# Optimization experiments

Hardware: AMD Instinct MI355X
Metric: run time of the kernel (lower is better)

Reference implementation:

```python
import jax, jax.numpy as jnp
import numpy as np

TOKEN_SELF_ATTN_VALUE = -50000.0


def setup_inputs() -> dict:
    key = jax.random.key(0)
    k1, k2, k3 = jax.random.split(key, 3)
    batch, seqlen, dim = 16, 4096, 64
    n_hashes, bucket_size = 8, 64
    n_buckets = seqlen // bucket_size  # 64
    qk = jax.random.normal(k1, (batch, seqlen, dim), dtype=jnp.float32)
    v = jax.random.normal(k2, (batch, seqlen, dim), dtype=jnp.float32)
    # random rotations for LSH hashing: (dim, n_hashes, n_buckets // 2)
    rotations = jax.random.normal(k3, (dim, n_hashes, n_buckets // 2), dtype=jnp.float32)
    return {"qk": qk, "v": v, "rotations": rotations}


def reference(qk, v, rotations):
    batch, seqlen, dim = qk.shape
    n_hashes = rotations.shape[1]
    n_buckets = 2 * rotations.shape[2]
    bucket_size = seqlen // n_buckets

    # ---- hash_vectors (rehash_each_round=True, no hash dropout) ----
    rotated = jnp.einsum('btf,fhi->bhti', qk, rotations)       # (b, h, t, nb/2)
    rotated = jnp.concatenate([rotated, -rotated], axis=-1)    # (b, h, t, nb)
    buckets = jnp.argmax(rotated, axis=-1)                     # (b, h, t)
    offsets = (jnp.arange(n_hashes) * n_buckets)[None, :, None]
    buckets = (buckets + offsets).reshape(batch, n_hashes * seqlen)

    # ---- sort tokens by (bucket, position) ----
    ticker = jnp.arange(n_hashes * seqlen)
    buckets_and_t = seqlen * buckets + (ticker % seqlen)[None, :]
    sticker = jnp.argsort(buckets_and_t, axis=-1)              # keys are unique
    undo_sort = jnp.argsort(sticker, axis=-1)
    st = sticker % seqlen                                      # original positions

    sqk = jnp.take_along_axis(qk, st[:, :, None], axis=1)      # (b, h*t, d)
    sv = jnp.take_along_axis(v, st[:, :, None], axis=1)

    chunk_size = n_hashes * n_buckets
    bq_t = st.reshape(batch, chunk_size, bucket_size)
    bqk = sqk.reshape(batch, chunk_size, bucket_size, dim)
    bv = sv.reshape(batch, chunk_size, bucket_size, dim)

    bq = bqk
    # F.normalize(p=2, eps=1e-12)
    bk = bqk / jnp.maximum(jnp.linalg.norm(bqk, axis=-1, keepdims=True), 1e-12)

    def look_one_back(x):
        return jnp.concatenate([x, jnp.roll(x, 1, axis=1)], axis=2)

    bk = look_one_back(bk)
    bv = look_one_back(bv)
    bkv_t = look_one_back(bq_t)

    dots = jnp.einsum('bcie,bcje->bcij', bq, bk) * (dim ** -0.5)  # (b, chunks, i, 2i)

    # self-attention mask (causal=False, no input masks by default)
    self_mask = bq_t[:, :, :, None] == bkv_t[:, :, None, :]
    dots = jnp.where(self_mask, TOKEN_SELF_ATTN_VALUE, dots)

    dots_logsumexp = jax.scipy.special.logsumexp(dots, axis=-1, keepdims=True)
    probs = jnp.exp(dots - dots_logsumexp)
    bo = jnp.einsum('bcij,bcje->bcie', probs, bv)

    so = bo.reshape(batch, -1, dim)                   # (b, h*t, d)
    slogits = dots_logsumexp.reshape(batch, -1)       # (b, h*t)

    # unsort back to original token order
    o = jnp.take_along_axis(so, undo_sort[:, :, None], axis=1)
    logits = jnp.take_along_axis(slogits, undo_sort, axis=1)

    o = o.reshape(batch, n_hashes, seqlen, dim)
    logits = logits.reshape(batch, n_hashes, seqlen, 1)

    # combine hash rounds weighted by their logsumexps
    w = jnp.exp(logits - jax.scipy.special.logsumexp(logits, axis=1, keepdims=True))
    out = jnp.sum(o * w, axis=1)                      # (b, t, d)
    return out
```

## Files before the change

### kernel.cpp

```cpp
#include <hip/hip_runtime.h>
#include <hip/hip_fp16.h>
#include <hip/hip_bf16.h>

#define BATCH  16
#define SEQ    4096
#define DIM    64
#define NHASH  8
#define NCHUNK 512
#define SB     72

typedef __attribute__((ext_vector_type(8))) short short8;
typedef __attribute__((ext_vector_type(4))) float floatx4;

__device__ __forceinline__ float trunc_hi(float a) {
    return __uint_as_float(__float_as_uint(a) & 0xffff0000u);
}
__device__ __forceinline__ unsigned pack_hi2(float a, float b) {
    return (__float_as_uint(a) >> 16) | (__float_as_uint(b) & 0xffff0000u);
}
__device__ __forceinline__ void hi16_store_cvt(const float* xs, short* dst) {
    union { __hip_bfloat162 h2[8]; uint4 u4[2]; } U;
#pragma unroll
    for (int u = 0; u < 8; ++u)
        U.h2[u] = __float22bfloat162_rn(make_float2(xs[2*u], xs[2*u + 1]));
    *(uint4*)(dst)     = U.u4[0];
    *(uint4*)(dst + 8) = U.u4[1];
}
__device__ __forceinline__ void split8_frag(const float* xs, short8* hi, short8* lo) {
    union { unsigned u[4]; short8 s; } H, L;
#pragma unroll
    for (int u = 0; u < 4; ++u) {
        float a = xs[2*u], b = xs[2*u + 1];
        H.u[u] = pack_hi2(a, b);
        L.u[u] = pack_hi2(a - trunc_hi(a), b - trunc_hi(b));
    }
    *hi = H.s; *lo = L.s;
}

__device__ __forceinline__ void argmax_store(
    const float* a, int gid, int h, int* __restrict__ buckets)
{
    float best = a[0]; int bi = 0;
#pragma unroll
    for (int i = 1; i < 32; ++i) { if (a[i] > best) { best = a[i]; bi = i; } }
#pragma unroll
    for (int i = 0; i < 32; ++i) { float nv = -a[i]; if (nv > best) { best = nv; bi = i + 32; } }
    int b = gid >> 12, t = gid & 4095;
    buckets[((size_t)b * NHASH + h) * SEQ + t] = bi;
}

__global__ __launch_bounds__(256, 4) void lsh_hash_kernel(
    const float* __restrict__ qk, const float* __restrict__ rot,
    int* __restrict__ buckets)
{
    __shared__ float rs[64 * 64];
    int tid = threadIdx.x;
    int tb   = blockIdx.x >> 2;
    int hsel = blockIdx.x & 3;

    {
        const float4* rg = (const float4*)rot;
#pragma unroll
        for (int j = 0; j < 4; ++j) {
            int idx4 = j * 256 + tid;
            int f = idx4 >> 4, r4 = idx4 & 15;
            ((float4*)rs)[idx4] = rg[f * 64 + hsel * 16 + r4];
        }
    }
    __syncthreads();

    int tt = tid & 127;
    int hh = tid >> 7;
    int gid0 = tb * 256 + tt;
    int gid1 = gid0 + 128;
    const float* q0 = qk + (size_t)gid0 * DIM;
    const float* q1 = qk + (size_t)gid1 * DIM;
    const float* rbase = rs + hh * 32;

    float a0[32], a1[32];
#pragma unroll
    for (int i = 0; i < 32; ++i) { a0[i] = 0.f; a1[i] = 0.f; }

#pragma unroll 1
    for (int ft = 0; ft < 8; ++ft) {
        float qa[8], qb[8];
        *(float4*)&qa[0] = *(const float4*)(q0 + ft * 8);
        *(float4*)&qa[4] = *(const float4*)(q0 + ft * 8 + 4);
        *(float4*)&qb[0] = *(const float4*)(q1 + ft * 8);
        *(float4*)&qb[4] = *(const float4*)(q1 + ft * 8 + 4);
#pragma unroll
        for (int f8 = 0; f8 < 8; ++f8) {
            const float* rp = rbase + (ft * 8 + f8) * 64;
            float x0 = qa[f8], x1 = qb[f8];
#pragma unroll
            for (int i = 0; i < 32; ++i) {
                float r = rp[i];
                a0[i] = fmaf(x0, r, a0[i]);
                a1[i] = fmaf(x1, r, a1[i]);
            }
        }
    }

    int h = hsel * 2 + hh;
    argmax_store(a0, gid0, h, buckets);
    argmax_store(a1, gid1, h, buckets);
}

__global__ __launch_bounds__(256) void lsh_sort_kernel(
    const int* __restrict__ buckets, int* __restrict__ st)
{
    __shared__ int hist[256 * 65];
    __shared__ int seg[256];
    __shared__ int base[64];

    int bh = blockIdx.x;
    int tid = threadIdx.x;
    int w = tid >> 6, lane = tid & 63;

    for (int i = tid; i < 256 * 65; i += 256) hist[i] = 0;

    int myb[16];
    {
        const int4* bp4 = (const int4*)(buckets + (size_t)bh * SEQ);
#pragma unroll
        for (int u4 = 0; u4 < 4; ++u4) {
            int4 bb = bp4[tid * 4 + u4];
            myb[u4*4+0] = bb.x; myb[u4*4+1] = bb.y;
            myb[u4*4+2] = bb.z; myb[u4*4+3] = bb.w;
        }
    }
    __syncthreads();
    int* hrow = &hist[tid * 65];
#pragma unroll
    for (int u = 0; u < 16; ++u) hrow[myb[u]] += 1;
    __syncthreads();

    {
        int run = 0;
        for (int tp = 0; tp < 64; ++tp) {
            int idx = (w * 64 + tp) * 65 + lane;
            int c0 = hist[idx];
            hist[idx] = run;
            run += c0;
        }
        seg[w * 64 + lane] = run;
    }
    __syncthreads();
    if (tid < 64) {
        int s0 = seg[lane], s1 = seg[64 + lane], s2 = seg[128 + lane], s3 = seg[192 + lane];
        seg[lane] = 0; seg[64 + lane] = s0;
        seg[128 + lane] = s0 + s1; seg[192 + lane] = s0 + s1 + s2;
        int tot = s0 + s1 + s2 + s3;
        int x = tot;
#pragma unroll
        for (int d = 1; d < 64; d <<= 1) {
            int y = __shfl_up(x, d, 64);
            if (lane >= d) x += y;
        }
        base[lane] = x - tot;
    }
    __syncthreads();

    int* op = st + (size_t)bh * SEQ;
#pragma unroll
    for (int u = 0; u < 16; ++u) {
        int bb = myb[u];
        int local = hrow[bb];
        hrow[bb] = local + 1;
        int pos = base[bb] + seg[w * 64 + bb] + local;
        op[pos] = tid * 16 + u;
    }
}

__global__ __launch_bounds__(256, 5) void lsh_attn_kernel(
    const float* __restrict__ qk, const float* __restrict__ v,
    const int* __restrict__ st, __half* __restrict__ Obuf, float* __restrict__ Dbuf)
{
    __shared__ short Khi[64 * SB];
    __shared__ short Vhi[64 * SB];
    __shared__ int   tk[64];
    __shared__ float lds_pad[2560];

    short* Phi = Khi;

    int tid  = threadIdx.x;
    {
        volatile float* vp = lds_pad;
        vp[tid] = 0.f;
    }
    int lane = tid & 63;
    int w    = tid >> 6;
    int quad = lane >> 4;
    int l15  = lane & 15;

    int B  = blockIdx.x;
    int bc = ((B & 7) << 10) | (B >> 3);
    int b = bc >> 9, c = bc & (NCHUNK - 1);
    int cm = (c + NCHUNK - 1) & (NCHUNK - 1);

    const int*   stb = st + (size_t)b * (NHASH * SEQ);
    const float* qkb = qk + (size_t)b * SEQ * DIM;
    const float* vb  = v  + (size_t)b * SEQ * DIM;

    short8 qH[2], qL[2];
    {
        int qt = stb[c * 64 + 16 * w + l15];
        const float* qp = qkb + (size_t)qt * DIM + 8 * quad;
        float xs[8];
#pragma unroll
        for (int kb = 0; kb < 2; ++kb) {
            *(float4*)&xs[0] = *(const float4*)(qp + 32 * kb);
            *(float4*)&xs[4] = *(const float4*)(qp + 32 * kb + 4);
            split8_frag(xs, &qH[kb], &qL[kb]);
        }
    }
    int tqr[4];
#pragma unroll
    for (int r = 0; r < 4; ++r) tqr[r] = stb[c * 64 + 16 * w + quad * 4 + r];

    float   Dacc[4] = {0.f, 0.f, 0.f, 0.f};
    floatx4 oacc[4];
#pragma unroll
    for (int a = 0; a < 4; ++a) oacc[a] = (floatx4){0.f, 0.f, 0.f, 0.f};

    for (int half = 0; half < 2; ++half) {
        int ck = half ? cm : c;
        __syncthreads();

        {
            int r = tid >> 2, s = tid & 3;
            int trow = stb[ck * 64 + r];
            if (s == 0) tk[r] = trow;
            const float4* k4 = (const float4*)(qkb + (size_t)trow * DIM + s * 16);
            float xs[16];
            *(float4*)&xs[0]  = k4[0];
            *(float4*)&xs[4]  = k4[1];
            *(float4*)&xs[8]  = k4[2];
            *(float4*)&xs[12] = k4[3];
            float ss = 0.f;
#pragma unroll
            for (int u = 0; u < 16; ++u) ss += xs[u] * xs[u];
            ss += __shfl_xor(ss, 1);
            ss += __shfl_xor(ss, 2);
            float sc = 1.0f / fmaxf(sqrtf(ss), 1e-12f);
#pragma unroll
            for (int u = 0; u < 16; ++u) xs[u] *= sc;
            hi16_store_cvt(xs, &Khi[r * SB + s * 16]);
        }
        {
            float xs[16];
#pragma unroll
            for (int u = 0; u < 16; ++u) {
                int trow = stb[ck * 64 + w * 16 + u];
                xs[u] = vb[(size_t)trow * DIM + lane];
            }
            hi16_store_cvt(xs, &Vhi[lane * SB + w * 16]);
        }
        __syncthreads();

        floatx4 dt[4];
#pragma unroll
        for (int jt = 0; jt < 4; ++jt) dt[jt] = (floatx4){0.f, 0.f, 0.f, 0.f};
#pragma unroll
        for (int kb = 0; kb < 2; ++kb) {
#pragma unroll
            for (int jt = 0; jt < 4; ++jt) {
                short8 bH = *(const short8*)&Khi[(16 * jt + l15) * SB + kb * 32 + quad * 8];
                dt[jt] = __builtin_amdgcn_mfma_f32_16x16x32_bf16(qH[kb], bH, dt[jt], 0, 0, 0);
                dt[jt] = __builtin_amdgcn_mfma_f32_16x16x32_bf16(qL[kb], bH, dt[jt], 0, 0, 0);
            }
        }
        __syncthreads();

#pragma unroll
        for (int jt = 0; jt < 4; ++jt) {
            int tkc = tk[16 * jt + l15];
#pragma unroll
            for (int r = 0; r < 4; ++r) {
                float p = (tqr[r] == tkc) ? 0.f : __expf(dt[jt][r] * 0.125f);
                Dacc[r] += p;
                int idx = (16 * w + quad * 4 + r) * SB + 16 * jt + l15;
                Phi[idx] = (short)((__float_as_uint(p) + 0x8000u) >> 16);
            }
        }

#pragma unroll
        for (int kb = 0; kb < 2; ++kb) {
            short8 aH = *(const short8*)&Phi[(16 * w + l15) * SB + kb * 32 + quad * 8];
#pragma unroll
            for (int a = 0; a < 4; ++a) {
                short8 bH = *(const short8*)&Vhi[(16 * a + l15) * SB + kb * 32 + quad * 8];
                oacc[a] = __builtin_amdgcn_mfma_f32_16x16x32_bf16(aH, bH, oacc[a], 0, 0, 0);
            }
        }
    }

    int h = c >> 6;
#pragma unroll
    for (int r = 0; r < 4; ++r) {
        int t = tqr[r];
        size_t rowb = ((size_t)(b * SEQ + t) * NHASH + h) * DIM;
#pragma unroll
        for (int a = 0; a < 4; ++a)
            Obuf[rowb + 16 * a + l15] = __float2half(oacc[a][r]);
    }
#pragma unroll
    for (int r = 0; r < 4; ++r) {
        float rs = Dacc[r];
        rs += __shfl_xor(rs, 1);
        rs += __shfl_xor(rs, 2);
        rs += __shfl_xor(rs, 4);
        rs += __shfl_xor(rs, 8);
        if (l15 == 0) Dbuf[(size_t)(b * SEQ + tqr[r]) * NHASH + h] = rs;
    }
}

__global__ __launch_bounds__(256) void lsh_combine_tok(
    const __half* __restrict__ Obuf, const float* __restrict__ Dbuf,
    float* __restrict__ out)
{
    int gid = blockIdx.x * 256 + threadIdx.x;
    int d4 = gid & 15;
    int bt = gid >> 4;

    const __half* op = Obuf + (size_t)bt * (NHASH * DIM) + d4 * 4;
    const float*  dp = Dbuf + (size_t)bt * NHASH;

    float4 n = make_float4(0.f, 0.f, 0.f, 0.f);
    float den = 0.f;
#pragma unroll
    for (int h = 0; h < NHASH; ++h) {
        uint2 u = *(const uint2*)(op + h * DIM);
        __half2 p01 = *(__half2*)&u.x;
        __half2 p23 = *(__half2*)&u.y;
        float2 f01 = __half22float2(p01);
        float2 f23 = __half22float2(p23);
        den += dp[h];
        n.x += f01.x; n.y += f01.y; n.z += f23.x; n.w += f23.y;
    }
    float invd = 1.0f / den;
    float4 r; r.x = n.x*invd; r.y = n.y*invd; r.z = n.z*invd; r.w = n.w*invd;
    ((float4*)out)[gid] = r;
}

extern "C" void kernel_launch(void* const* d_in, const int* in_sizes, int n_in,
                              void* d_out, int out_size, void* d_ws, size_t ws_size,
                              hipStream_t stream)
{
    const float* qk  = (const float*)d_in[0];
    const float* v   = (const float*)d_in[1];
    const float* rot = (const float*)d_in[2];
    float* out = (float*)d_out;

    char* w = (char*)d_ws;
    int*    buckets = (int*)(w);
    int*    st      = (int*)(w + 2097152);
    __half* Obuf    = (__half*)(w + 4194304);
    float*  Dbuf    = (float*)(w + 4194304 + 67108864);

    lsh_hash_kernel<<<1024, 256, 0, stream>>>(qk, rot, buckets);
    lsh_sort_kernel<<<128, 256, 0, stream>>>(buckets, st);
    lsh_attn_kernel<<<8192, 256, 0, stream>>>(qk, v, st, Obuf, Dbuf);
    lsh_combine_tok<<<4096, 256, 0, stream>>>(Obuf, Dbuf, out);
}
```

Before: 201.4 us.

## Drop split-bf16 QK precision, transpose dot MFMA, pass P through registers via shuffles

The Q fragment is now a single rounded bf16 value instead of a hi/lo split, which halves the QK^T MFMA count. The dot product is computed transposed (K as the A operand), so each lane holds one query's scores. The probability tile is then redistributed across lanes with shuffles instead of being written to and read back from LDS, which removes a __syncthreads and LDS traffic, and the row-sum reduction becomes simpler. The cost is lower QK precision, which could hurt accuracy, plus extra shuffle instructions.

```diff
diff --git a/kernel.cpp b/kernel.cpp
--- a/kernel.cpp
+++ b/kernel.cpp
@@ -12,12 +12,6 @@
 typedef __attribute__((ext_vector_type(8))) short short8;
 typedef __attribute__((ext_vector_type(4))) float floatx4;
 
-__device__ __forceinline__ float trunc_hi(float a) {
-    return __uint_as_float(__float_as_uint(a) & 0xffff0000u);
-}
-__device__ __forceinline__ unsigned pack_hi2(float a, float b) {
-    return (__float_as_uint(a) >> 16) | (__float_as_uint(b) & 0xffff0000u);
-}
 __device__ __forceinline__ void hi16_store_cvt(const float* xs, short* dst) {
     union { __hip_bfloat162 h2[8]; uint4 u4[2]; } U;
 #pragma unroll
@@ -26,15 +20,10 @@
     *(uint4*)(dst)     = U.u4[0];
     *(uint4*)(dst + 8) = U.u4[1];
 }
-__device__ __forceinline__ void split8_frag(const float* xs, short8* hi, short8* lo) {
-    union { unsigned u[4]; short8 s; } H, L;
-#pragma unroll
-    for (int u = 0; u < 4; ++u) {
-        float a = xs[2*u], b = xs[2*u + 1];
-        H.u[u] = pack_hi2(a, b);
-        L.u[u] = pack_hi2(a - trunc_hi(a), b - trunc_hi(b));
-    }
-    *hi = H.s; *lo = L.s;
+__device__ __forceinline__ unsigned pk_bf16(float a, float b) {
+    union { __hip_bfloat162 h2; unsigned u; } U;
+    U.h2 = __float22bfloat162_rn(make_float2(a, b));
+    return U.u;
 }
 
 __device__ __forceinline__ void argmax_store(
@@ -181,8 +170,6 @@
     __shared__ int   tk[64];
     __shared__ float lds_pad[2560];
 
-    short* Phi = Khi;
-
     int tid  = threadIdx.x;
     {
         volatile float* vp = lds_pad;
@@ -202,26 +189,35 @@
     const float* qkb = qk + (size_t)b * SEQ * DIM;
     const float* vb  = v  + (size_t)b * SEQ * DIM;
 
-    short8 qH[2], qL[2];
-    {
-        int qt = stb[c * 64 + 16 * w + l15];
+    short8 qH[2];
+    int qt;
+    {
+        qt = stb[c * 64 + 16 * w + l15];
         const float* qp = qkb + (size_t)qt * DIM + 8 * quad;
-        float xs[8];
 #pragma unroll
         for (int kb = 0; kb < 2; ++kb) {
+            float xs[8];
             *(float4*)&xs[0] = *(const float4*)(qp + 32 * kb);
             *(float4*)&xs[4] = *(const float4*)(qp + 32 * kb + 4);
-            split8_frag(xs, &qH[kb], &qL[kb]);
+            union { __hip_bfloat162 h2[4]; short8 s; } Uq;
+#pragma unroll
+            for (int u = 0; u < 4; ++u)
+                Uq.h2[u] = __float22bfloat162_rn(make_float2(xs[2*u], xs[2*u + 1]));
+            qH[kb] = Uq.s;
         }
     }
     int tqr[4];
 #pragma unroll
     for (int r = 0; r < 4; ++r) tqr[r] = stb[c * 64 + 16 * w + quad * 4 + r];
 
-    float   Dacc[4] = {0.f, 0.f, 0.f, 0.f};
+    float   Dacc = 0.f;
     floatx4 oacc[4];
 #pragma unroll
     for (int a = 0; a < 4; ++a) oacc[a] = (floatx4){0.f, 0.f, 0.f, 0.f};
+
+    int sA = l15 + ((lane & 16) ? 32 : 0);
+    int sB = sA + 16;
+    bool qhi = (lane >= 32);
 
     for (int half = 0; half < 2; ++half) {
         int ck = half ? cm : c;
@@ -265,32 +261,43 @@
         for (int kb = 0; kb < 2; ++kb) {
 #pragma unroll
             for (int jt = 0; jt < 4; ++jt) {
-                short8 bH = *(const short8*)&Khi[(16 * jt + l15) * SB + kb * 32 + quad * 8];
-                dt[jt] = __builtin_amdgcn_mfma_f32_16x16x32_bf16(qH[kb], bH, dt[jt], 0, 0, 0);
-                dt[jt] = __builtin_amdgcn_mfma_f32_16x16x32_bf16(qL[kb], bH, dt[jt], 0, 0, 0);
+                short8 kf = *(const short8*)&Khi[(16 * jt + l15) * SB + kb * 32 + quad * 8];
+                dt[jt] = __builtin_amdgcn_mfma_f32_16x16x32_bf16(kf, qH[kb], dt[jt], 0, 0, 0);
             }
         }
-        __syncthreads();
-
+
+        unsigned U[8];
 #pragma unroll
         for (int jt = 0; jt < 4; ++jt) {
-            int tkc = tk[16 * jt + l15];
-#pragma unroll
-            for (int r = 0; r < 4; ++r) {
-                float p = (tqr[r] == tkc) ? 0.f : __expf(dt[jt][r] * 0.125f);
-                Dacc[r] += p;
-                int idx = (16 * w + quad * 4 + r) * SB + 16 * jt + l15;
-                Phi[idx] = (short)((__float_as_uint(p) + 0x8000u) >> 16);
-            }
+            int4 tkq = *(const int4*)&tk[16 * jt + quad * 4];
+            float p0 = (qt == tkq.x) ? 0.f : __expf(dt[jt][0] * 0.125f);
+            float p1 = (qt == tkq.y) ? 0.f : __expf(dt[jt][1] * 0.125f);
+            float p2 = (qt == tkq.z) ? 0.f : __expf(dt[jt][2] * 0.125f);
+            float p3 = (qt == tkq.w) ? 0.f : __expf(dt[jt][3] * 0.125f);
+            Dacc += (p0 + p1) + (p2 + p3);
+            U[2*jt]     = pk_bf16(p0, p1);
+            U[2*jt + 1] = pk_bf16(p2, p3);
         }
 
 #pragma unroll
         for (int kb = 0; kb < 2; ++kb) {
-            short8 aH = *(const short8*)&Phi[(16 * w + l15) * SB + kb * 32 + quad * 8];
+            unsigned xA0 = (unsigned)__shfl((int)U[4*kb + 0], sA, 64);
+            unsigned yA0 = (unsigned)__shfl((int)U[4*kb + 2], sA, 64);
+            unsigned xA1 = (unsigned)__shfl((int)U[4*kb + 1], sA, 64);
+            unsigned yA1 = (unsigned)__shfl((int)U[4*kb + 3], sA, 64);
+            unsigned xB0 = (unsigned)__shfl((int)U[4*kb + 0], sB, 64);
+            unsigned yB0 = (unsigned)__shfl((int)U[4*kb + 2], sB, 64);
+            unsigned xB1 = (unsigned)__shfl((int)U[4*kb + 1], sB, 64);
+            unsigned yB1 = (unsigned)__shfl((int)U[4*kb + 3], sB, 64);
+            union { uint4 u; short8 s; } A;
+            A.u.x = qhi ? yA0 : xA0;
+            A.u.y = qhi ? yA1 : xA1;
+            A.u.z = qhi ? yB0 : xB0;
+            A.u.w = qhi ? yB1 : xB1;
 #pragma unroll
             for (int a = 0; a < 4; ++a) {
                 short8 bH = *(const short8*)&Vhi[(16 * a + l15) * SB + kb * 32 + quad * 8];
-                oacc[a] = __builtin_amdgcn_mfma_f32_16x16x32_bf16(aH, bH, oacc[a], 0, 0, 0);
+                oacc[a] = __builtin_amdgcn_mfma_f32_16x16x32_bf16(A.s, bH, oacc[a], 0, 0, 0);
             }
         }
     }
@@ -304,15 +311,9 @@
         for (int a = 0; a < 4; ++a)
             Obuf[rowb + 16 * a + l15] = __float2half(oacc[a][r]);
     }
-#pragma unroll
-    for (int r = 0; r < 4; ++r) {
-        float rs = Dacc[r];
-        rs += __shfl_xor(rs, 1);
-        rs += __shfl_xor(rs, 2);
-        rs += __shfl_xor(rs, 4);
-        rs += __shfl_xor(rs, 8);
-        if (l15 == 0) Dbuf[(size_t)(b * SEQ + tqr[r]) * NHASH + h] = rs;
-    }
+    Dacc += __shfl_xor(Dacc, 16);
+    Dacc += __shfl_xor(Dacc, 32);
+    if (lane < 16) Dbuf[(size_t)(b * SEQ + qt) * NHASH + h] = Dacc;
 }
 
 __global__ __launch_bounds__(256) void lsh_combine_tok(
```

After: 198.5 us. Within noise of the previous version (-1.4%).
